# Performance work log

Hardware: AMD Instinct MI355X
Metric: run time of the kernel (lower is better)

The kernel has to match this reference:

```python
import jax, jax.numpy as jnp
import numpy as np

NUM_CLASSES = 80
CLS_W, BOX_W, OBJ_W = 0.5, 7.5, 1.0
CENTER_RADIUS = 2.5
LABEL_SMOOTH = 0.0
WARMUP = min(1.0, (0 + 1) / 3)  # current_epoch=0, warmup_epochs=3
EPS = 1e-7


def _make_points(img=640, strides=(8, 16, 32)):
    pts, strs = [], []
    for s in strides:
        n = img // s
        ys, xs = np.meshgrid(np.arange(n), np.arange(n), indexing='ij')
        p = np.stack([(xs + 0.5) * s, (ys + 0.5) * s], -1).reshape(-1, 2)
        pts.append(p)
        strs.append(np.full(p.shape[0], s))
    return (np.concatenate(pts).astype(np.float32),
            np.concatenate(strs).astype(np.float32))


def _rand_boxes(key, shape, img=640.0):
    k1, k2 = jax.random.split(key)
    c = jax.random.uniform(k1, shape + (2,), minval=50.0, maxval=img - 50.0)
    half = jax.random.uniform(k2, shape + (2,), minval=8.0, maxval=120.0)
    return jnp.concatenate([c - half, c + half], axis=-1)


def setup_inputs() -> dict:
    key = jax.random.key(0)
    ks = jax.random.split(key, 6)
    B, P, G, C = 16, 8400, 64, NUM_CLASSES
    points_np, strides_np = _make_points()
    return {
        'pred_cls': jax.random.normal(ks[0], (B, P, C), jnp.float32),
        'pred_box': jax.random.normal(ks[1], (B, P, 4), jnp.float32),
        'pred_obj': jax.random.normal(ks[2], (B, P, 1), jnp.float32),
        'decoded_boxes': _rand_boxes(ks[3], (B, P)),
        'points': jnp.asarray(points_np),
        'strides': jnp.asarray(strides_np),
        'gt_boxes': _rand_boxes(ks[4], (B, G)),
        'gt_labels': jax.random.randint(ks[5], (B, G), 0, C, jnp.int32),
    }


def _ciou_loss(b1, b2):
    # b1, b2: [..., 4] in x1y1x2y2. Returns 1 - CIoU per box.
    x1, y1, x2, y2 = b1[..., 0], b1[..., 1], b1[..., 2], b1[..., 3]
    gx1, gy1, gx2, gy2 = b2[..., 0], b2[..., 1], b2[..., 2], b2[..., 3]
    w1, h1 = x2 - x1, y2 - y1
    w2, h2 = gx2 - gx1, gy2 - gy1
    inter = (jnp.clip(jnp.minimum(x2, gx2) - jnp.maximum(x1, gx1), 0.0) *
             jnp.clip(jnp.minimum(y2, gy2) - jnp.maximum(y1, gy1), 0.0))
    union = w1 * h1 + w2 * h2 - inter + EPS
    iou = inter / union
    cw = jnp.maximum(x2, gx2) - jnp.minimum(x1, gx1)
    ch = jnp.maximum(y2, gy2) - jnp.minimum(y1, gy1)
    c2 = cw * cw + ch * ch + EPS
    rho2 = ((x1 + x2 - gx1 - gx2) ** 2 + (y1 + y2 - gy1 - gy2) ** 2) * 0.25
    v = (4.0 / (jnp.pi ** 2)) * (jnp.arctan(w2 / (h2 + EPS)) -
                                 jnp.arctan(w1 / (h1 + EPS))) ** 2
    alpha = v / (1.0 - iou + v + EPS)
    return 1.0 - (iou - rho2 / c2 - alpha * v)


def _assign(points, strides, gt_boxes):
    # points [P,2], strides [P], gt_boxes [B,G,4] -> fg [B,P], idx [B,P]
    px = points[None, :, None, 0]                 # [1,P,1]
    py = points[None, :, None, 1]
    gx1 = gt_boxes[:, None, :, 0]                 # [B,1,G]
    gy1 = gt_boxes[:, None, :, 1]
    gx2 = gt_boxes[:, None, :, 2]
    gy2 = gt_boxes[:, None, :, 3]
    deltas = jnp.stack([px - gx1, py - gy1, gx2 - px, gy2 - py], -1)  # [B,P,G,4]
    inside_box = jnp.min(deltas, -1) > 0
    cx, cy = (gx1 + gx2) * 0.5, (gy1 + gy2) * 0.5
    radii = strides[None, :, None] * CENTER_RADIUS
    cdeltas = jnp.stack([px - (cx - radii), py - (cy - radii),
                         cx + radii - px, cy + radii - py], -1)
    inside_center = jnp.min(cdeltas, -1) > 0
    fits = jnp.max(deltas, -1) <= strides[None, :, None] * 8.0
    match = inside_box & inside_center & fits
    fallback = inside_box & inside_center
    match = jnp.where(jnp.any(match, -1, keepdims=True), match, fallback)
    areas = ((gt_boxes[..., 2] - gt_boxes[..., 0]) *
             (gt_boxes[..., 3] - gt_boxes[..., 1]))[:, None, :]  # [B,1,G]
    cand = jnp.where(match, areas, jnp.inf)
    matched_idx = jnp.argmin(cand, -1)                            # [B,P]
    fg = jnp.isfinite(jnp.min(cand, -1))
    return fg, matched_idx


def _bce_mean(logits, targets):
    return jnp.mean(jnp.maximum(logits, 0.0) - logits * targets +
                    jnp.log1p(jnp.exp(-jnp.abs(logits))))


def reference(pred_cls, pred_box, pred_obj, decoded_boxes, points, strides,
              gt_boxes, gt_labels):
    dtype = pred_cls.dtype
    fg, midx = _assign(points, strides, gt_boxes)                 # [B,P]
    matched_boxes = jnp.take_along_axis(
        gt_boxes, midx[:, :, None].repeat(4, axis=2), axis=1)      # [B,P,4]
    matched_labels = jnp.take_along_axis(gt_labels, midx, axis=1)  # [B,P]

    # cls target: one-hot (with optional smoothing) at fg points, zeros elsewhere
    one_hot = jax.nn.one_hot(matched_labels, NUM_CLASSES, dtype=dtype)
    if LABEL_SMOOTH > 0.0:
        one_hot = one_hot * (1.0 - LABEL_SMOOTH) + LABEL_SMOOTH / NUM_CLASSES
    cls_target = jnp.where(fg[..., None], one_hot, 0.0)

    # sanitize predicted boxes
    pb = jnp.nan_to_num(decoded_boxes, nan=0.0, posinf=1000.0, neginf=0.0)
    pb = jnp.clip(pb, -1000.0, 1000.0)
    px1, py1 = pb[..., 0], pb[..., 1]
    px2 = jnp.maximum(px1 + 0.001, pb[..., 2])
    py2 = jnp.maximum(py1 + 0.001, pb[..., 3])
    pb = jnp.stack([px1, py1, px2, py2], -1)

    ciou = _ciou_loss(pb, matched_boxes)                          # [B,P]
    ciou = jnp.clip(jnp.nan_to_num(ciou, nan=1.0, posinf=1.0, neginf=1.0), 0.0, 2.0)

    num_fg = jnp.sum(fg.astype(dtype))
    normalizer = jnp.maximum(num_fg, 1.0)
    loss_box = jnp.sum(jnp.where(fg, ciou, 0.0)) / normalizer
    loss_box = jnp.minimum(jnp.nan_to_num(loss_box), 10.0)

    obj_target = jax.lax.stop_gradient(
        jnp.where(fg, jnp.clip(1.0 - ciou, 0.0, 1.0), 0.0))

    loss_cls = jnp.minimum(jnp.nan_to_num(_bce_mean(pred_cls, cls_target)), 10.0)
    loss_obj = jnp.minimum(jnp.nan_to_num(
        _bce_mean(pred_obj[..., 0], obj_target)), 10.0)

    loss_total = CLS_W * loss_cls + (BOX_W * WARMUP) * loss_box + OBJ_W * loss_obj
    loss_total = jnp.minimum(jnp.nan_to_num(loss_total), 10.0)
    return jnp.stack([loss_total, loss_cls, loss_box, loss_obj])
```

## Files before the change

kernel.cpp:

```cpp
#include <hip/hip_runtime.h>
#include <cmath>

#define NCLS 80
#define NB 16
#define NP 8400
#define NG 64
#define CHUNKS 33
#define PBLK (NB * CHUNKS)
#define NBLK 1024
#define N4 (NB * NP * NCLS / 4)
#define EPSF 1e-7f

__device__ __forceinline__ float softplus_bce(float l) {
    float t = __expf(-fabsf(l));
    return fmaxf(l, 0.f) + __logf(1.f + t);
}

__device__ __forceinline__ float sanitize_box(float x) {
    if (isnan(x)) return 0.f;
    if (isinf(x)) x = (x > 0.f) ? 1000.f : 0.f;
    return fminf(fmaxf(x, -1000.f), 1000.f);
}

__global__ __launch_bounds__(256) void k1_main(
    const float* __restrict__ pred_cls, const float* __restrict__ pred_obj,
    const float4* __restrict__ decoded, const float2* __restrict__ points,
    const float* __restrict__ strides, const float4* __restrict__ gt_boxes,
    const int* __restrict__ gt_labels, double* __restrict__ part)
{
    const int bid = blockIdx.x, tid = threadIdx.x;

    double v0 = 0.0, v1 = 0.0, v2 = 0.0, v3 = 0.0, v4 = 0.0;

    {
        const float4* cls4 = (const float4*)pred_cls;
        for (int i = bid * 256 + tid; i < N4; i += NBLK * 256) {
            float4 c = cls4[i];
            float s = softplus_bce(c.x) + softplus_bce(c.y) +
                      softplus_bce(c.z) + softplus_bce(c.w);
            v0 += (double)s;
        }
    }

    if (bid < PBLK) {
        __shared__ float4 gbox[NG];
        __shared__ float garea[NG];
        __shared__ int glab[NG];

        const int b = bid / CHUNKS;
        const int chunk = bid % CHUNKS;
        const int p = chunk * 256 + tid;

        if (tid < NG) {
            float4 gb = gt_boxes[b * NG + tid];
            gbox[tid] = gb;
            garea[tid] = (gb.z - gb.x) * (gb.w - gb.y);
            glab[tid] = gt_labels[b * NG + tid];
        }
        __syncthreads();

        if (p < NP) {
            float2 pt = points[p];
            const float px = pt.x, py = pt.y;
            const float s = strides[p];
            const float r = s * 2.5f;
            const float fit_thr = s * 8.0f;

            unsigned long long match = 0ull, fallback = 0ull;
            #pragma unroll 4
            for (int g = 0; g < NG; ++g) {
                float4 gb = gbox[g];
                float d0 = px - gb.x, d1 = py - gb.y, d2 = gb.z - px, d3 = gb.w - py;
                float dmin = fminf(fminf(d0, d1), fminf(d2, d3));
                float dmax = fmaxf(fmaxf(d0, d1), fmaxf(d2, d3));
                bool ib = dmin > 0.f;
                float cx = (gb.x + gb.z) * 0.5f, cy = (gb.y + gb.w) * 0.5f;
                float c0 = px - (cx - r), c1 = py - (cy - r);
                float c2 = cx + r - px, c3 = cy + r - py;
                float cmin = fminf(fminf(c0, c1), fminf(c2, c3));
                bool fb = ib && (cmin > 0.f);
                bool m = fb && (dmax <= fit_thr);
                unsigned long long bit = 1ull << g;
                if (m) match |= bit;
                if (fb) fallback |= bit;
            }
            unsigned long long mask = match ? match : fallback;

            float lo = pred_obj[b * NP + p];
            float tobj = 0.f;

            if (mask) {
                int best = 0; float bestA = INFINITY;
                unsigned long long mm = mask;
                while (mm) {
                    int g = __ffsll((long long)mm) - 1;
                    mm &= mm - 1;
                    float a = garea[g];
                    if (a < bestA) { bestA = a; best = g; }
                }
                v1 = 1.0;

                float4 db = decoded[(size_t)b * NP + p];
                float x1 = sanitize_box(db.x);
                float y1 = sanitize_box(db.y);
                float x2 = fmaxf(x1 + 0.001f, sanitize_box(db.z));
                float y2 = fmaxf(y1 + 0.001f, sanitize_box(db.w));

                float4 g4 = gbox[best];
                float gx1 = g4.x, gy1 = g4.y, gx2 = g4.z, gy2 = g4.w;

                float w1 = x2 - x1, h1 = y2 - y1;
                float w2 = gx2 - gx1, h2 = gy2 - gy1;
                float iw = fmaxf(fminf(x2, gx2) - fmaxf(x1, gx1), 0.f);
                float ih = fmaxf(fminf(y2, gy2) - fmaxf(y1, gy1), 0.f);
                float inter = iw * ih;
                float uni = w1 * h1 + w2 * h2 - inter + EPSF;
                float iou = inter / uni;
                float cw = fmaxf(x2, gx2) - fminf(x1, gx1);
                float ch = fmaxf(y2, gy2) - fminf(y1, gy1);
                float c2d = cw * cw + ch * ch + EPSF;
                float dx = x1 + x2 - gx1 - gx2, dy = y1 + y2 - gy1 - gy2;
                float rho2 = (dx * dx + dy * dy) * 0.25f;
                float da = atanf(w2 / (h2 + EPSF)) - atanf(w1 / (h1 + EPSF));
                float vv = 0.40528473456935108577551785283891f * da * da;
                float alpha = vv / (1.f - iou + vv + EPSF);
                float ciou = 1.f - (iou - rho2 / c2d - alpha * vv);
                if (isnan(ciou) || isinf(ciou)) ciou = 1.f;
                ciou = fminf(fmaxf(ciou, 0.f), 2.f);
                v2 = (double)ciou;
                tobj = fminf(fmaxf(1.f - ciou, 0.f), 1.f);

                v4 = (double)pred_cls[((size_t)b * NP + p) * NCLS + glab[best]];
            }
            v3 = (double)(softplus_bce(lo) - lo * tobj);
        }
    }

    __shared__ double sh[5][4];
    double vals[5] = {v0, v1, v2, v3, v4};
    for (int k = 0; k < 5; ++k) {
        double v = vals[k];
        for (int off = 32; off; off >>= 1) v += __shfl_down(v, off, 64);
        if ((tid & 63) == 0) sh[k][tid >> 6] = v;
    }
    __syncthreads();
    if (tid == 0) {
        #pragma unroll
        for (int k = 0; k < 5; ++k)
            part[(size_t)k * NBLK + bid] = sh[k][0] + sh[k][1] + sh[k][2] + sh[k][3];
    }
}

__global__ __launch_bounds__(256) void k2_finalize(
    const double* __restrict__ part, float* __restrict__ out)
{
    double a[5] = {0, 0, 0, 0, 0};
    for (int i = threadIdx.x; i < NBLK; i += 256) {
        #pragma unroll
        for (int k = 0; k < 5; ++k) a[k] += part[(size_t)k * NBLK + i];
    }
    __shared__ double sh2[4];
    __shared__ double tot[5];
    for (int k = 0; k < 5; ++k) {
        double v = a[k];
        for (int off = 32; off; off >>= 1) v += __shfl_down(v, off, 64);
        __syncthreads();
        if ((threadIdx.x & 63) == 0) sh2[threadIdx.x >> 6] = v;
        __syncthreads();
        if (threadIdx.x == 0) tot[k] = sh2[0] + sh2[1] + sh2[2] + sh2[3];
    }
    __syncthreads();
    if (threadIdx.x == 0) {
        double cls_sum = tot[0], fg_sum = tot[1], box_sum = tot[2],
               obj_sum = tot[3], corr_sum = tot[4];

        float loss_cls = (float)((cls_sum - corr_sum) /
                                 (double)((size_t)NB * NP * NCLS));
        if (isnan(loss_cls)) loss_cls = 0.f;
        loss_cls = fminf(loss_cls, 10.f);

        float numfg = (float)fg_sum;
        float norm = fmaxf(numfg, 1.f);
        float loss_box = (float)box_sum / norm;
        if (isnan(loss_box)) loss_box = 0.f;
        loss_box = fminf(loss_box, 10.f);

        float loss_obj = (float)(obj_sum / (double)(NB * NP));
        if (isnan(loss_obj)) loss_obj = 0.f;
        loss_obj = fminf(loss_obj, 10.f);

        float total = 0.5f * loss_cls + 2.5f * loss_box + loss_obj;
        if (isnan(total)) total = 0.f;
        total = fminf(total, 10.f);

        out[0] = total; out[1] = loss_cls; out[2] = loss_box; out[3] = loss_obj;
    }
}

extern "C" void kernel_launch(void* const* d_in, const int* in_sizes, int n_in,
                              void* d_out, int out_size, void* d_ws, size_t ws_size,
                              hipStream_t stream) {
    const float*  pred_cls  = (const float*)d_in[0];
    const float*  pred_obj  = (const float*)d_in[2];
    const float4* decoded   = (const float4*)d_in[3];
    const float2* points    = (const float2*)d_in[4];
    const float*  strides   = (const float*)d_in[5];
    const float4* gt_boxes  = (const float4*)d_in[6];
    const int*    gt_labels = (const int*)d_in[7];

    double* part = (double*)d_ws;

    k1_main<<<NBLK, 256, 0, stream>>>(
        pred_cls, pred_obj, decoded, points, strides, gt_boxes, gt_labels, part);
    k2_finalize<<<1, 256, 0, stream>>>(part, (float*)d_out);
}
```

Before: 28.86 us.

## Split class-BCE streaming and point matching into separate block roles

Result: no change. 28.65 us (-0.7%).

```diff
diff --git a/kernel.cpp b/kernel.cpp
--- a/kernel.cpp
+++ b/kernel.cpp
@@ -7,13 +7,18 @@
 #define NG 64
 #define CHUNKS 33
 #define PBLK (NB * CHUNKS)
-#define NBLK 1024
+#define CBLK 2625
 #define N4 (NB * NP * NCLS / 4)
 #define EPSF 1e-7f
 
 __device__ __forceinline__ float softplus_bce(float l) {
     float t = __expf(-fabsf(l));
     return fmaxf(l, 0.f) + __logf(1.f + t);
+}
+
+__device__ __forceinline__ float sp4(float4 c) {
+    return (softplus_bce(c.x) + softplus_bce(c.y)) +
+           (softplus_bce(c.z) + softplus_bce(c.w));
 }
 
 __device__ __forceinline__ float sanitize_box(float x) {
@@ -26,119 +31,127 @@
     const float* __restrict__ pred_cls, const float* __restrict__ pred_obj,
     const float4* __restrict__ decoded, const float2* __restrict__ points,
     const float* __restrict__ strides, const float4* __restrict__ gt_boxes,
-    const int* __restrict__ gt_labels, double* __restrict__ part)
+    const int* __restrict__ gt_labels,
+    double* __restrict__ clsPart, double* __restrict__ pPart)
 {
     const int bid = blockIdx.x, tid = threadIdx.x;
 
-    double v0 = 0.0, v1 = 0.0, v2 = 0.0, v3 = 0.0, v4 = 0.0;
-
-    {
+    if (bid >= PBLK) {
+        const int cb = bid - PBLK;
         const float4* cls4 = (const float4*)pred_cls;
-        for (int i = bid * 256 + tid; i < N4; i += NBLK * 256) {
-            float4 c = cls4[i];
-            float s = softplus_bce(c.x) + softplus_bce(c.y) +
-                      softplus_bce(c.z) + softplus_bce(c.w);
-            v0 += (double)s;
+        const int base = cb * 1024 + tid;
+        float4 c0 = cls4[base];
+        float4 c1 = cls4[base + 256];
+        float4 c2 = cls4[base + 512];
+        float4 c3 = cls4[base + 768];
+        double acc = (double)sp4(c0) + (double)sp4(c1) +
+                     (double)sp4(c2) + (double)sp4(c3);
+
+        __shared__ double shc[4];
+        for (int off = 32; off; off >>= 1) acc += __shfl_down(acc, off, 64);
+        if ((tid & 63) == 0) shc[tid >> 6] = acc;
+        __syncthreads();
+        if (tid == 0) clsPart[cb] = shc[0] + shc[1] + shc[2] + shc[3];
+        return;
+    }
+
+    __shared__ float4 gbox[NG];
+    __shared__ float garea[NG];
+    __shared__ int glab[NG];
+
+    const int b = bid / CHUNKS;
+    const int chunk = bid % CHUNKS;
+    const int p = chunk * 256 + tid;
+
+    if (tid < NG) {
+        float4 gb = gt_boxes[b * NG + tid];
+        gbox[tid] = gb;
+        garea[tid] = (gb.z - gb.x) * (gb.w - gb.y);
+        glab[tid] = gt_labels[b * NG + tid];
+    }
+    __syncthreads();
+
+    double v1 = 0.0, v2 = 0.0, v3 = 0.0, v4 = 0.0;
+
+    if (p < NP) {
+        float2 pt = points[p];
+        const float px = pt.x, py = pt.y;
+        const float s = strides[p];
+        const float r = s * 2.5f;
+        const float fit_thr = s * 8.0f;
+
+        unsigned long long match = 0ull, fallback = 0ull;
+        #pragma unroll 4
+        for (int g = 0; g < NG; ++g) {
+            float4 gb = gbox[g];
+            float d0 = px - gb.x, d1 = py - gb.y, d2 = gb.z - px, d3 = gb.w - py;
+            float dmin = fminf(fminf(d0, d1), fminf(d2, d3));
+            float dmax = fmaxf(fmaxf(d0, d1), fmaxf(d2, d3));
+            bool ib = dmin > 0.f;
+            float cx = (gb.x + gb.z) * 0.5f, cy = (gb.y + gb.w) * 0.5f;
+            float c0 = px - (cx - r), c1 = py - (cy - r);
+            float c2 = cx + r - px, c3 = cy + r - py;
+            float cmin = fminf(fminf(c0, c1), fminf(c2, c3));
+            bool fb = ib && (cmin > 0.f);
+            bool m = fb && (dmax <= fit_thr);
+            unsigned long long bit = 1ull << g;
+            if (m) match |= bit;
+            if (fb) fallback |= bit;
         }
-    }
-
-    if (bid < PBLK) {
-        __shared__ float4 gbox[NG];
-        __shared__ float garea[NG];
-        __shared__ int glab[NG];
-
-        const int b = bid / CHUNKS;
-        const int chunk = bid % CHUNKS;
-        const int p = chunk * 256 + tid;
-
-        if (tid < NG) {
-            float4 gb = gt_boxes[b * NG + tid];
-            gbox[tid] = gb;
-            garea[tid] = (gb.z - gb.x) * (gb.w - gb.y);
-            glab[tid] = gt_labels[b * NG + tid];
+        unsigned long long mask = match ? match : fallback;
+
+        float lo = pred_obj[b * NP + p];
+        float tobj = 0.f;
+
+        if (mask) {
+            int best = 0; float bestA = INFINITY;
+            unsigned long long mm = mask;
+            while (mm) {
+                int g = __ffsll((long long)mm) - 1;
+                mm &= mm - 1;
+                float a = garea[g];
+                if (a < bestA) { bestA = a; best = g; }
+            }
+            v1 = 1.0;
+
+            float4 db = decoded[(size_t)b * NP + p];
+            float x1 = sanitize_box(db.x);
+            float y1 = sanitize_box(db.y);
+            float x2 = fmaxf(x1 + 0.001f, sanitize_box(db.z));
+            float y2 = fmaxf(y1 + 0.001f, sanitize_box(db.w));
+
+            float4 g4 = gbox[best];
+            float gx1 = g4.x, gy1 = g4.y, gx2 = g4.z, gy2 = g4.w;
+
+            float w1 = x2 - x1, h1 = y2 - y1;
+            float w2 = gx2 - gx1, h2 = gy2 - gy1;
+            float iw = fmaxf(fminf(x2, gx2) - fmaxf(x1, gx1), 0.f);
+            float ih = fmaxf(fminf(y2, gy2) - fmaxf(y1, gy1), 0.f);
+            float inter = iw * ih;
+            float uni = w1 * h1 + w2 * h2 - inter + EPSF;
+            float iou = inter / uni;
+            float cw = fmaxf(x2, gx2) - fminf(x1, gx1);
+            float ch = fmaxf(y2, gy2) - fminf(y1, gy1);
+            float c2d = cw * cw + ch * ch + EPSF;
+            float dx = x1 + x2 - gx1 - gx2, dy = y1 + y2 - gy1 - gy2;
+            float rho2 = (dx * dx + dy * dy) * 0.25f;
+            float da = atanf(w2 / (h2 + EPSF)) - atanf(w1 / (h1 + EPSF));
+            float vv = 0.40528473456935108577551785283891f * da * da;
+            float alpha = vv / (1.f - iou + vv + EPSF);
+            float ciou = 1.f - (iou - rho2 / c2d - alpha * vv);
+            if (isnan(ciou) || isinf(ciou)) ciou = 1.f;
+            ciou = fminf(fmaxf(ciou, 0.f), 2.f);
+            v2 = (double)ciou;
+            tobj = fminf(fmaxf(1.f - ciou, 0.f), 1.f);
+
+            v4 = (double)pred_cls[((size_t)b * NP + p) * NCLS + glab[best]];
         }
-        __syncthreads();
-
-        if (p < NP) {
-            float2 pt = points[p];
-            const float px = pt.x, py = pt.y;
-            const float s = strides[p];
-            const float r = s * 2.5f;
-            const float fit_thr = s * 8.0f;
-
-            unsigned long long match = 0ull, fallback = 0ull;
-            #pragma unroll 4
-            for (int g = 0; g < NG; ++g) {
-                float4 gb = gbox[g];
-                float d0 = px - gb.x, d1 = py - gb.y, d2 = gb.z - px, d3 = gb.w - py;
-                float dmin = fminf(fminf(d0, d1), fminf(d2, d3));
-                float dmax = fmaxf(fmaxf(d0, d1), fmaxf(d2, d3));
-                bool ib = dmin > 0.f;
-                float cx = (gb.x + gb.z) * 0.5f, cy = (gb.y + gb.w) * 0.5f;
-                float c0 = px - (cx - r), c1 = py - (cy - r);
-                float c2 = cx + r - px, c3 = cy + r - py;
-                float cmin = fminf(fminf(c0, c1), fminf(c2, c3));
-                bool fb = ib && (cmin > 0.f);
-                bool m = fb && (dmax <= fit_thr);
-                unsigned long long bit = 1ull << g;
-                if (m) match |= bit;
-                if (fb) fallback |= bit;
-            }
-            unsigned long long mask = match ? match : fallback;
-
-            float lo = pred_obj[b * NP + p];
-            float tobj = 0.f;
-
-            if (mask) {
-                int best = 0; float bestA = INFINITY;
-                unsigned long long mm = mask;
-                while (mm) {
-                    int g = __ffsll((long long)mm) - 1;
-                    mm &= mm - 1;
-                    float a = garea[g];
-                    if (a < bestA) { bestA = a; best = g; }
-                }
-                v1 = 1.0;
-
-                float4 db = decoded[(size_t)b * NP + p];
-                float x1 = sanitize_box(db.x);
-                float y1 = sanitize_box(db.y);
-                float x2 = fmaxf(x1 + 0.001f, sanitize_box(db.z));
-                float y2 = fmaxf(y1 + 0.001f, sanitize_box(db.w));
-
-                float4 g4 = gbox[best];
-                float gx1 = g4.x, gy1 = g4.y, gx2 = g4.z, gy2 = g4.w;
-
-                float w1 = x2 - x1, h1 = y2 - y1;
-                float w2 = gx2 - gx1, h2 = gy2 - gy1;
-                float iw = fmaxf(fminf(x2, gx2) - fmaxf(x1, gx1), 0.f);
-                float ih = fmaxf(fminf(y2, gy2) - fmaxf(y1, gy1), 0.f);
-                float inter = iw * ih;
-                float uni = w1 * h1 + w2 * h2 - inter + EPSF;
-                float iou = inter / uni;
-                float cw = fmaxf(x2, gx2) - fminf(x1, gx1);
-                float ch = fmaxf(y2, gy2) - fminf(y1, gy1);
-                float c2d = cw * cw + ch * ch + EPSF;
-                float dx = x1 + x2 - gx1 - gx2, dy = y1 + y2 - gy1 - gy2;
-                float rho2 = (dx * dx + dy * dy) * 0.25f;
-                float da = atanf(w2 / (h2 + EPSF)) - atanf(w1 / (h1 + EPSF));
-                float vv = 0.40528473456935108577551785283891f * da * da;
-                float alpha = vv / (1.f - iou + vv + EPSF);
-                float ciou = 1.f - (iou - rho2 / c2d - alpha * vv);
-                if (isnan(ciou) || isinf(ciou)) ciou = 1.f;
-                ciou = fminf(fmaxf(ciou, 0.f), 2.f);
-                v2 = (double)ciou;
-                tobj = fminf(fmaxf(1.f - ciou, 0.f), 1.f);
-
-                v4 = (double)pred_cls[((size_t)b * NP + p) * NCLS + glab[best]];
-            }
-            v3 = (double)(softplus_bce(lo) - lo * tobj);
-        }
-    }
-
-    __shared__ double sh[5][4];
-    double vals[5] = {v0, v1, v2, v3, v4};
-    for (int k = 0; k < 5; ++k) {
+        v3 = (double)(softplus_bce(lo) - lo * tobj);
+    }
+
+    __shared__ double sh[4][4];
+    double vals[4] = {v1, v2, v3, v4};
+    for (int k = 0; k < 4; ++k) {
         double v = vals[k];
         for (int off = 32; off; off >>= 1) v += __shfl_down(v, off, 64);
         if ((tid & 63) == 0) sh[k][tid >> 6] = v;
@@ -146,31 +159,34 @@
     __syncthreads();
     if (tid == 0) {
         #pragma unroll
-        for (int k = 0; k < 5; ++k)
-            part[(size_t)k * NBLK + bid] = sh[k][0] + sh[k][1] + sh[k][2] + sh[k][3];
+        for (int k = 0; k < 4; ++k)
+            pPart[(size_t)k * PBLK + bid] = sh[k][0] + sh[k][1] + sh[k][2] + sh[k][3];
     }
 }
 
 __global__ __launch_bounds__(256) void k2_finalize(
-    const double* __restrict__ part, float* __restrict__ out)
+    const double* __restrict__ clsPart, const double* __restrict__ pPart,
+    float* __restrict__ out)
 {
+    const int tid = threadIdx.x;
     double a[5] = {0, 0, 0, 0, 0};
-    for (int i = threadIdx.x; i < NBLK; i += 256) {
-        #pragma unroll
-        for (int k = 0; k < 5; ++k) a[k] += part[(size_t)k * NBLK + i];
-    }
+    for (int i = tid; i < CBLK; i += 256) a[0] += clsPart[i];
+    #pragma unroll
+    for (int k = 0; k < 4; ++k)
+        for (int i = tid; i < PBLK; i += 256) a[1 + k] += pPart[(size_t)k * PBLK + i];
+
     __shared__ double sh2[4];
     __shared__ double tot[5];
     for (int k = 0; k < 5; ++k) {
         double v = a[k];
         for (int off = 32; off; off >>= 1) v += __shfl_down(v, off, 64);
         __syncthreads();
-        if ((threadIdx.x & 63) == 0) sh2[threadIdx.x >> 6] = v;
+        if ((tid & 63) == 0) sh2[tid >> 6] = v;
         __syncthreads();
-        if (threadIdx.x == 0) tot[k] = sh2[0] + sh2[1] + sh2[2] + sh2[3];
+        if (tid == 0) tot[k] = sh2[0] + sh2[1] + sh2[2] + sh2[3];
     }
     __syncthreads();
-    if (threadIdx.x == 0) {
+    if (tid == 0) {
         double cls_sum = tot[0], fg_sum = tot[1], box_sum = tot[2],
                obj_sum = tot[3], corr_sum = tot[4];
 
@@ -208,9 +224,11 @@
     const float4* gt_boxes  = (const float4*)d_in[6];
     const int*    gt_labels = (const int*)d_in[7];
 
-    double* part = (double*)d_ws;
-
-    k1_main<<<NBLK, 256, 0, stream>>>(
-        pred_cls, pred_obj, decoded, points, strides, gt_boxes, gt_labels, part);
-    k2_finalize<<<1, 256, 0, stream>>>(part, (float*)d_out);
-}
+    double* clsPart = (double*)d_ws;
+    double* pPart   = clsPart + CBLK;
+
+    k1_main<<<PBLK + CBLK, 256, 0, stream>>>(
+        pred_cls, pred_obj, decoded, points, strides, gt_boxes, gt_labels,
+        clsPart, pPart);
+    k2_finalize<<<1, 256, 0, stream>>>(clsPart, pPart, (float*)d_out);
+}
```
